# Optimization experiments

Measured on AMD Instinct MI355X. Metric: run time of the kernel, lower is better.

## Reference

```python
import jax, jax.numpy as jnp
import numpy as np
from jax.scipy.special import logsumexp

B, T, D, H, K = 64, 800, 80, 128, 39  # batch, frames, feat dim, LSTM hidden/dir, num phones


def setup_inputs() -> dict:
    key = jax.random.key(0)
    ks = jax.random.split(key, 16)
    s = 0.1
    inp = {
        "features": jax.random.normal(ks[0], (B, T, D), jnp.float32),
        "lengths": jax.random.randint(ks[1], (B,), T // 2, T + 1, dtype=jnp.int32),
        "labels": jax.random.randint(ks[2], (B, T), 0, K, dtype=jnp.int32),
        # BiLSTM params (PyTorch layout: W_ih (4H,D), W_hh (4H,H); gate order i,f,g,o)
        "Wih_f": jax.random.normal(ks[3], (4 * H, D), jnp.float32) * s,
        "Whh_f": jax.random.normal(ks[4], (4 * H, H), jnp.float32) * s,
        "bih_f": jax.random.normal(ks[5], (4 * H,), jnp.float32) * s,
        "bhh_f": jax.random.normal(ks[6], (4 * H,), jnp.float32) * s,
        "Wih_b": jax.random.normal(ks[7], (4 * H, D), jnp.float32) * s,
        "Whh_b": jax.random.normal(ks[8], (4 * H, H), jnp.float32) * s,
        "bih_b": jax.random.normal(ks[9], (4 * H,), jnp.float32) * s,
        "bhh_b": jax.random.normal(ks[10], (4 * H,), jnp.float32) * s,
        # emission projection Linear(2H -> K)
        "Wp": jax.random.normal(ks[11], (K, 2 * H), jnp.float32) * s,
        "bp": jax.random.normal(ks[12], (K,), jnp.float32) * s,
        # CRF params (pytorch-crf init: U(-0.1, 0.1))
        "start_t": jax.random.uniform(ks[13], (K,), jnp.float32, -0.1, 0.1),
        "end_t": jax.random.uniform(ks[14], (K,), jnp.float32, -0.1, 0.1),
        "trans": jax.random.uniform(ks[15], (K, K), jnp.float32, -0.1, 0.1),
    }
    return inp


def _lstm(x, Wih, Whh, bih, bhh, reverse):
    """Single-direction LSTM over padded batch. x: (B,T,D) -> (B,T,H)."""
    nB, nT, _ = x.shape
    nH = Whh.shape[1]
    xW = jnp.swapaxes(x @ Wih.T + (bih + bhh), 0, 1)  # (T,B,4H)

    def step(carry, g):
        h, c = carry
        g = g + h @ Whh.T
        i, f, gg, o = jnp.split(g, 4, axis=-1)
        c = jax.nn.sigmoid(f) * c + jax.nn.sigmoid(i) * jnp.tanh(gg)
        h = jax.nn.sigmoid(o) * jnp.tanh(c)
        return (h, c), h

    init = (jnp.zeros((nB, nH), x.dtype), jnp.zeros((nB, nH), x.dtype))
    _, hs = jax.lax.scan(step, init, xW, reverse=reverse)
    return jnp.swapaxes(hs, 0, 1)  # (B,T,H)


def _crf_nll(emissions, labels, lengths, start_t, end_t, trans):
    """pytorch-crf: -mean log-likelihood. emissions (B,T,K), labels (B,T)."""
    nB, nT, nK = emissions.shape
    mask = (jnp.arange(nT)[None, :] < lengths[:, None])  # (B,T)
    mf = mask.astype(emissions.dtype)
    bidx = jnp.arange(nB)

    # --- numerator: score of gold path ---
    num = start_t[labels[:, 0]] + emissions[bidx, 0, labels[:, 0]]
    tr = trans[labels[:, :-1], labels[:, 1:]]  # (B,T-1)
    em = jnp.take_along_axis(emissions[:, 1:], labels[:, 1:, None], axis=2)[..., 0]
    num = num + ((tr + em) * mf[:, 1:]).sum(axis=1)
    last_tags = jnp.take_along_axis(labels, (lengths - 1)[:, None], axis=1)[:, 0]
    num = num + end_t[last_tags]

    # --- denominator: forward algorithm ---
    alpha0 = start_t[None, :] + emissions[:, 0]  # (B,K)
    em_rest = jnp.swapaxes(emissions[:, 1:], 0, 1)  # (T-1,B,K)
    m_rest = jnp.swapaxes(mask[:, 1:], 0, 1)  # (T-1,B)

    def step(alpha, inputs):
        em_t, m_t = inputs
        nxt = logsumexp(alpha[:, :, None] + trans[None] + em_t[:, None, :], axis=1)
        return jnp.where(m_t[:, None], nxt, alpha), None

    alpha, _ = jax.lax.scan(step, alpha0, (em_rest, m_rest))
    denom = logsumexp(alpha + end_t[None, :], axis=1)

    return -(num - denom).mean()


def reference(features, lengths, labels, Wih_f, Whh_f, bih_f, bhh_f,
              Wih_b, Whh_b, bih_b, bhh_b, Wp, bp, start_t, end_t, trans):
    h_f = _lstm(features, Wih_f, Whh_f, bih_f, bhh_f, reverse=False)
    h_b = _lstm(features, Wih_b, Whh_b, bih_b, bhh_b, reverse=True)
    hidden = jnp.concatenate([h_f, h_b], axis=-1)  # (B,T,2H)
    emissions = hidden @ Wp.T + bp  # (B,T,K)
    return _crf_nll(emissions, labels, lengths, start_t, end_t, trans)
```

## Files before the change

### kernel.cpp

```cpp
#include <hip/hip_runtime.h>
#include <cstddef>
#include <cstdint>

#define B_ 64
#define T_ 800
#define D_ 80
#define H_ 128
#define K_ 39
#define BT_ (B_ * T_)

typedef _Float16 h2_t  __attribute__((ext_vector_type(2)));
typedef _Float16 f16x8 __attribute__((ext_vector_type(8)));
typedef float    f32x4 __attribute__((ext_vector_type(4)));
typedef uint32_t u32x4 __attribute__((ext_vector_type(4)));

__device__ __forceinline__ float fdot2_(h2_t a, h2_t b, float c) {
#if __has_builtin(__builtin_amdgcn_fdot2)
  return __builtin_amdgcn_fdot2(a, b, c, false);
#else
  return c + (float)a.x * (float)b.x + (float)a.y * (float)b.y;
#endif
}

__device__ __forceinline__ h2_t asH2u_(uint32_t u) { return __builtin_bit_cast(h2_t, u); }

__device__ __forceinline__ float sigf_(float x)  { return 1.0f / (1.0f + __expf(-x)); }
__device__ __forceinline__ float tanhf_(float x) { return 2.0f / (1.0f + __expf(-2.0f * x)) - 1.0f; }

__device__ __forceinline__ float laneb_(float v, int lane) {
  return __builtin_bit_cast(float, __builtin_amdgcn_readlane(__builtin_bit_cast(int, v), lane));
}
__device__ __forceinline__ uint32_t lanebu_(uint32_t v, int lane) {
  return (uint32_t)__builtin_amdgcn_readlane((int)v, lane);
}

__device__ __forceinline__ float dppswap1_(float v) {
  return __builtin_bit_cast(float,
    __builtin_amdgcn_mov_dpp(__builtin_bit_cast(int, v), 0xB1, 0xF, 0xF, true));
}

__device__ __forceinline__ void barrier_lds_() {
  asm volatile("s_waitcnt lgkmcnt(0)" ::: "memory");
  __builtin_amdgcn_s_barrier();
}

__device__ __forceinline__ void rows_of_(int tid, int& unit, int& role, int& r0, int& r1) {
  const int w = tid >> 6, L = tid & 63;
  unit = w * 32 + (L >> 1);
  role = L & 1;
  r0 = role * H_ + unit;
  r1 = 2 * H_ + role * H_ + unit;
}

__global__ __launch_bounds__(256, 1)
void xw_kernel(const float* __restrict__ x,
               const float* __restrict__ Wih_f, const float* __restrict__ Wih_b,
               _Float16* __restrict__ xw)
{
  const int dir = blockIdx.x & 1;
  const int mc  = blockIdx.x >> 1;
  const float* W = dir ? Wih_b : Wih_f;

  const int tid  = threadIdx.x;
  const int w    = tid >> 6;
  const int lane = tid & 63;
  const int lm   = lane & 15;
  const int quad = lane >> 4;
  const int selw = w >> 1;
  const int rolw = w & 1;

  f16x8 Bf[8][3];
  #pragma unroll
  for (int nt = 0; nt < 8; ++nt) {
    const int r = w * 128 + nt * 16 + lm;
    #pragma unroll
    for (int kt = 0; kt < 3; ++kt) {
      const int kb = kt * 32 + quad * 8;
      #pragma unroll
      for (int j = 0; j < 8; ++j) {
        const int k = kb + j;
        Bf[nt][kt][j] = (k < D_) ? (_Float16)W[(size_t)r * D_ + k] : (_Float16)0.0f;
      }
    }
  }

  __shared__ alignas(16) _Float16 xs[128 * 96];
  for (int i = tid; i < 128 * 96; i += 256) xs[i] = (_Float16)0.0f;

  for (int cc = 0; cc < 4; ++cc) {
    const int base = mc * 512 + cc * 128;
    __syncthreads();
    {
      const float4* src = (const float4*)(x + (size_t)base * D_);
      for (int i = tid; i < 128 * D_ / 4; i += 256) {
        float4 v = src[i];
        const int row = i / 20, col = (i % 20) * 4;
        h2_t p0, p1;
        p0.x = (_Float16)v.x; p0.y = (_Float16)v.y;
        p1.x = (_Float16)v.z; p1.y = (_Float16)v.w;
        uint2 pk;
        pk.x = __builtin_bit_cast(uint32_t, p0);
        pk.y = __builtin_bit_cast(uint32_t, p1);
        *(uint2*)&xs[row * 96 + col] = pk;
      }
    }
    __syncthreads();

    #pragma unroll
    for (int mt = 0; mt < 8; ++mt) {
      f16x8 Af[3];
      #pragma unroll
      for (int kt = 0; kt < 3; ++kt)
        Af[kt] = *(const f16x8*)&xs[(mt * 16 + lm) * 96 + kt * 32 + quad * 8];

      f32x4 acc[8];
      #pragma unroll
      for (int nt = 0; nt < 8; ++nt) acc[nt] = (f32x4){0.f, 0.f, 0.f, 0.f};
      #pragma unroll
      for (int kt = 0; kt < 3; ++kt)
        #pragma unroll
        for (int nt = 0; nt < 8; ++nt)
          acc[nt] = __builtin_amdgcn_mfma_f32_16x16x32_f16(Af[kt], Bf[nt][kt], acc[nt], 0, 0, 0);

      #pragma unroll
      for (int nt = 0; nt < 8; ++nt) {
        const int unit = nt * 16 + lm;
        const int ptid = (unit >> 5) * 64 + (unit & 31) * 2 + rolw;
        #pragma unroll
        for (int rg = 0; rg < 4; ++rg) {
          const int bt = base + mt * 16 + quad * 4 + rg;
          xw[((size_t)dir * BT_ + bt) * 512 + ptid * 2 + selw] = (_Float16)acc[nt][rg];
        }
      }
    }
  }
}

template<int USE_XW>
__global__ __launch_bounds__(256, 1)
void lstm_kernel(const float* __restrict__ x,
                 const float* __restrict__ Wih_f, const float* __restrict__ Whh_f,
                 const float* __restrict__ bih_f, const float* __restrict__ bhh_f,
                 const float* __restrict__ Wih_b, const float* __restrict__ Whh_b,
                 const float* __restrict__ bih_b, const float* __restrict__ bhh_b,
                 const _Float16* __restrict__ xw,
                 _Float16* __restrict__ hcat)
{
  const int bb  = blockIdx.x & 63;
  const int dir = blockIdx.x >> 6;
  const float* Whh = dir ? Whh_b : Whh_f;
  const float* Wih = dir ? Wih_b : Wih_f;
  const float* bih = dir ? bih_b : bih_f;
  const float* bhh = dir ? bhh_b : bhh_f;

  const int tid  = threadIdx.x;
  const int lane = tid & 63;
  int unit, role, r0, r1; rows_of_(tid, unit, role, r0, r1);
  const float qc1 = role ? 1.0f : 2.0f;
  const float qc0 = role ? 0.0f : -1.0f;

  h2_t w0[64], w1[64];
  #pragma unroll
  for (int j = 0; j < 64; ++j) {
    float2 a = *(const float2*)(Whh + (size_t)r0 * H_ + 2 * j);
    float2 d = *(const float2*)(Whh + (size_t)r1 * H_ + 2 * j);
    w0[j].x = (_Float16)a.x; w0[j].y = (_Float16)a.y;
    w1[j].x = (_Float16)d.x; w1[j].y = (_Float16)d.y;
  }
  h2_t wx0[40], wx1[40];
  if (!USE_XW) {
    #pragma unroll
    for (int i = 0; i < 40; ++i) {
      float2 a = *(const float2*)(Wih + (size_t)r0 * D_ + 2 * i);
      float2 d = *(const float2*)(Wih + (size_t)r1 * D_ + 2 * i);
      wx0[i].x = (_Float16)a.x; wx0[i].y = (_Float16)a.y;
      wx1[i].x = (_Float16)d.x; wx1[i].y = (_Float16)d.y;
    }
  }
  const float bias0 = bih[r0] + bhh[r0];
  const float bias1 = bih[r1] + bhh[r1];

  __shared__ alignas(16) _Float16 hsf[2][H_];
  __shared__ uint32_t xs2[2][64];

  if (tid < H_) hsf[0][tid] = (_Float16)0.0f;
  if (!USE_XW && tid < 64) { xs2[0][tid] = 0u; xs2[1][tid] = 0u; }
  float c = 0.0f;

  const uint32_t* xwdu = (const uint32_t*)xw + ((size_t)dir * BT_ + (size_t)bb * T_) * 256;
  const float*    xb   = x + (size_t)bb * T_ * D_;
  _Float16*       hb   = hcat + (size_t)bb * T_ * (2 * H_) + dir * H_;

  uint32_t xwA = 0u, xwB = 0u;
  h2_t xpend; xpend.x = (_Float16)0.f; xpend.y = (_Float16)0.f;
  {
    const int tq0 = dir ? (T_ - 1) : 0;
    const int tq1 = dir ? (T_ - 2) : 1;
    if (USE_XW) {
      xwA = xwdu[(size_t)tq0 * 256 + tid];
      xwB = xwdu[(size_t)tq1 * 256 + tid];
    } else if (tid < 40) {
      float2 v0 = *(const float2*)(xb + (size_t)tq0 * D_ + 2 * tid);
      h2_t p; p.x = (_Float16)v0.x; p.y = (_Float16)v0.y;
      xs2[0][tid] = __builtin_bit_cast(uint32_t, p);
      float2 v1 = *(const float2*)(xb + (size_t)tq1 * D_ + 2 * tid);
      xpend.x = (_Float16)v1.x; xpend.y = (_Float16)v1.y;
    }
  }
  __syncthreads();

  auto step = [&](int tt, int par, uint32_t& xwreg) {
    const int t = dir ? (T_ - 1 - tt) : tt;
    float a0, a1, b0, b1;
    if (USE_XW) {
      const h2_t xv = asH2u_(xwreg);
      a0 = bias0 + (float)xv.x;
      b0 = bias1 + (float)xv.y;
      a1 = 0.f; b1 = 0.f;
      const int ttc = (tt + 2 < T_) ? (tt + 2) : (T_ - 1);
      const int tq2 = dir ? (T_ - 1 - ttc) : ttc;
      xwreg = xwdu[(size_t)tq2 * 256 + tid];
    } else {
      a0 = bias0; a1 = 0.f; b0 = bias1; b1 = 0.f;
      if (tid < 40) {
        xs2[par ^ 1][tid] = __builtin_bit_cast(uint32_t, xpend);
        const int ttc = (tt + 2 < T_) ? (tt + 2) : (T_ - 1);
        const int tq2 = dir ? (T_ - 1 - ttc) : ttc;
        float2 v = *(const float2*)(xb + (size_t)tq2 * D_ + 2 * tid);
        xpend.x = (_Float16)v.x; xpend.y = (_Float16)v.y;
      }
      uint32_t xreg = xs2[par][lane];
      #pragma unroll
      for (int j = 0; j < 40; j += 2) {
        h2_t q0 = asH2u_(lanebu_(xreg, j));
        h2_t q1 = asH2u_(lanebu_(xreg, j + 1));
        a0 = fdot2_(wx0[j],     q0, a0); b0 = fdot2_(wx1[j],     q0, b0);
        a1 = fdot2_(wx0[j + 1], q1, a1); b1 = fdot2_(wx1[j + 1], q1, b1);
      }
    }

    const u32x4* hq = (const u32x4*)hsf[par];
    #pragma unroll
    for (int g = 0; g < 16; ++g) {
      const u32x4 hv = hq[g];
      a0 = fdot2_(w0[4 * g + 0], asH2u_(hv[0]), a0);
      b0 = fdot2_(w1[4 * g + 0], asH2u_(hv[0]), b0);
      a1 = fdot2_(w0[4 * g + 1], asH2u_(hv[1]), a1);
      b1 = fdot2_(w1[4 * g + 1], asH2u_(hv[1]), b1);
      a0 = fdot2_(w0[4 * g + 2], asH2u_(hv[2]), a0);
      b0 = fdot2_(w1[4 * g + 2], asH2u_(hv[2]), b0);
      a1 = fdot2_(w0[4 * g + 3], asH2u_(hv[3]), a1);
      b1 = fdot2_(w1[4 * g + 3], asH2u_(hv[3]), b1);
    }
    const float ga = a0 + a1;
    const float gb = b0 + b1;

    const float sg = sigf_(ga);
    const float qv = fmaf(qc1, sigf_(qc1 * gb), qc0);
    const float ex = dppswap1_(sg * qv);
    c = fmaf(sg, c, ex);
    const float hn = qv * tanhf_(c);
    if (role) {
      hsf[par ^ 1][unit] = (_Float16)hn;
      hb[(size_t)t * (2 * H_) + unit] = (_Float16)hn;
    }
    barrier_lds_();
  };

  for (int tb = 0; tb < T_; tb += 2) {
    step(tb,     0, xwA);
    step(tb + 1, 1, xwB);
  }
}

__global__ __launch_bounds__(256, 1)
void emis_kernel(const _Float16* __restrict__ hcat,
                 const float* __restrict__ Wp, const float* __restrict__ bp,
                 float* __restrict__ em)
{
  const int tid  = threadIdx.x;
  const int w    = tid >> 6;
  const int lane = tid & 63;
  const int lm   = lane & 15;
  const int quad = lane >> 4;

  f16x8 Bf[3][8];
  float bias[3];
  #pragma unroll
  for (int nt = 0; nt < 3; ++nt) {
    const int n = nt * 16 + lm;
    const bool valid = n < K_;
    bias[nt] = valid ? bp[n] : 0.0f;
    #pragma unroll
    for (int kt = 0; kt < 8; ++kt) {
      const int kb = kt * 32 + quad * 8;
      #pragma unroll
      for (int j = 0; j < 8; ++j)
        Bf[nt][kt][j] = valid ? (_Float16)Wp[(size_t)n * 256 + kb + j] : (_Float16)0.0f;
    }
  }

  #pragma unroll
  for (int q = 0; q < 4; ++q) {
    const int mt  = blockIdx.x * 16 + w * 4 + q;
    const int bt0 = mt * 16;

    f16x8 Af[8];
    const _Float16* ab = hcat + ((size_t)bt0 + lm) * 256;
    #pragma unroll
    for (int kt = 0; kt < 8; ++kt)
      Af[kt] = *(const f16x8*)(ab + kt * 32 + quad * 8);

    f32x4 acc[3];
    #pragma unroll
    for (int nt = 0; nt < 3; ++nt) acc[nt] = (f32x4){0.f, 0.f, 0.f, 0.f};
    #pragma unroll
    for (int kt = 0; kt < 8; ++kt)
      #pragma unroll
      for (int nt = 0; nt < 3; ++nt)
        acc[nt] = __builtin_amdgcn_mfma_f32_16x16x32_f16(Af[kt], Bf[nt][kt], acc[nt], 0, 0, 0);

    #pragma unroll
    for (int nt = 0; nt < 3; ++nt) {
      const int n = nt * 16 + lm;
      if (n < K_) {
        #pragma unroll
        for (int rg = 0; rg < 4; ++rg) {
          const int row = bt0 + quad * 4 + rg;
          em[(size_t)row * K_ + n] = acc[nt][rg] + bias[nt];
        }
      }
    }
  }
}

__global__ __launch_bounds__(256)
void crf_dn_kernel(const float* __restrict__ em,
                   const int* __restrict__ labels, const int* __restrict__ lengths,
                   const float* __restrict__ start_t, const float* __restrict__ end_t,
                   const float* __restrict__ trans,
                   float* __restrict__ dn)
{
  const int b    = blockIdx.x;
  const int tid  = threadIdx.x;
  const int wv   = tid >> 6;
  const int lane = tid & 63;
  const int len  = lengths[b];
  const float* emb = em + (size_t)b * T_ * K_;

  __shared__ float s_num[3];
  __shared__ float s_den;

  if (wv == 0) {
    float et[K_];
    #pragma unroll
    for (int j = 0; j < K_; ++j)
      et[j] = (lane < K_) ? __expf(trans[j * K_ + lane]) : 0.0f;

    float a0 = (lane < K_) ? (start_t[lane] + emb[lane]) : -1e30f;
    float m = a0;
    #pragma unroll
    for (int off = 32; off > 0; off >>= 1) m = fmaxf(m, __shfl_xor(m, off));
    float v = __expf(a0 - m);
    float off_acc = m;

    auto ldc = [&](int t) -> float {
      const int tc = (t < len) ? t : (len - 1);
      return (lane < K_) ? emb[(size_t)tc * K_ + lane] : 0.0f;
    };

    float eA = ldc(1), eB = ldc(2), eC = ldc(3), eD = ldc(4);
    float eE = ldc(5), eF = ldc(6), eG = ldc(7), eH = ldc(8);

    auto stepden = [&](float& ereg, int tt) {
      const float emc = ereg;
      ereg = ldc(tt + 8);
      if (tt < len) {
        const float pv = v;
        float s0 = 0.f, s1 = 0.f, s2 = 0.f, s3 = 0.f;
        #pragma unroll
        for (int j = 0; j < 36; j += 4) {
          s0 = fmaf(laneb_(pv, j),     et[j],     s0);
          s1 = fmaf(laneb_(pv, j + 1), et[j + 1], s1);
          s2 = fmaf(laneb_(pv, j + 2), et[j + 2], s2);
          s3 = fmaf(laneb_(pv, j + 3), et[j + 3], s3);
        }
        s0 = fmaf(laneb_(pv, 36), et[36], s0);
        s1 = fmaf(laneb_(pv, 37), et[37], s1);
        s2 = fmaf(laneb_(pv, 38), et[38], s2);
        v = ((s0 + s1) + (s2 + s3)) * __expf(emc);
        if ((tt & 1) == 0) {
          const float sc = laneb_(v, 0);
          v *= 1.0f / sc;
          off_acc += __logf(sc);
        }
      }
    };

    for (int t = 1; t < len; t += 8) {
      stepden(eA, t);     stepden(eB, t + 1);
      stepden(eC, t + 2); stepden(eD, t + 3);
      stepden(eE, t + 4); stepden(eF, t + 5);
      stepden(eG, t + 6); stepden(eH, t + 7);
    }

    float w = (lane < K_) ? v * __expf(end_t[lane]) : 0.0f;
    #pragma unroll
    for (int off = 32; off > 0; off >>= 1) w += __shfl_xor(w, off);
    if (lane == 0) s_den = off_acc + __logf(w);
  } else {
    const int idx = tid - 64;
    float acc = 0.0f;
    for (int t = 1 + idx; t < len; t += 192) {
      const int lp = labels[b * T_ + t - 1];
      const int lc = labels[b * T_ + t];
      acc += trans[lp * K_ + lc] + emb[(size_t)t * K_ + lc];
    }
    if (tid == 64) {
      const int l0 = labels[b * T_];
      const int ll = labels[b * T_ + len - 1];
      acc += start_t[l0] + emb[l0] + end_t[ll];
    }
    #pragma unroll
    for (int off = 32; off > 0; off >>= 1) acc += __shfl_xor(acc, off);
    if (lane == 0) s_num[wv - 1] = acc;
  }
  __syncthreads();
  if (tid == 0) dn[b] = s_den - (s_num[0] + s_num[1] + s_num[2]);
}

__global__ void finalize_kernel(const float* __restrict__ dn, float* __restrict__ out)
{
  const int tid = threadIdx.x;
  float v = dn[tid];
  #pragma unroll
  for (int off = 32; off > 0; off >>= 1) v += __shfl_down(v, off);
  if (tid == 0) out[0] = v * (1.0f / 64.0f);
}

extern "C" void kernel_launch(void* const* d_in, const int* in_sizes, int n_in,
                              void* d_out, int out_size, void* d_ws, size_t ws_size,
                              hipStream_t stream)
{
  (void)in_sizes; (void)n_in; (void)out_size;
  const float* features = (const float*)d_in[0];
  const int*   lengths  = (const int*)d_in[1];
  const int*   labels   = (const int*)d_in[2];
  const float* Wih_f = (const float*)d_in[3];
  const float* Whh_f = (const float*)d_in[4];
  const float* bih_f = (const float*)d_in[5];
  const float* bhh_f = (const float*)d_in[6];
  const float* Wih_b = (const float*)d_in[7];
  const float* Whh_b = (const float*)d_in[8];
  const float* bih_b = (const float*)d_in[9];
  const float* bhh_b = (const float*)d_in[10];
  const float* Wp      = (const float*)d_in[11];
  const float* bp      = (const float*)d_in[12];
  const float* start_t = (const float*)d_in[13];
  const float* end_t   = (const float*)d_in[14];
  const float* trans   = (const float*)d_in[15];
  float* out = (float*)d_out;

  char* wsc = (char*)d_ws;
  _Float16* hcatH = (_Float16*)wsc;
  float*    em    = (float*)(wsc + 26214400);
  float*    dn    = (float*)(wsc + 26214400 + 7987200);
  _Float16* xwH   = (_Float16*)(wsc + 34202112);
  const bool big  = ws_size >= (size_t)34202112 + 104857600;

  if (big) {
    hipLaunchKernelGGL(xw_kernel, dim3(200), dim3(256), 0, stream,
                       features, Wih_f, Wih_b, xwH);
    hipLaunchKernelGGL((lstm_kernel<1>), dim3(2 * B_), dim3(256), 0, stream,
                       features, Wih_f, Whh_f, bih_f, bhh_f,
                       Wih_b, Whh_b, bih_b, bhh_b, xwH, hcatH);
  } else {
    hipLaunchKernelGGL((lstm_kernel<0>), dim3(2 * B_), dim3(256), 0, stream,
                       features, Wih_f, Whh_f, bih_f, bhh_f,
                       Wih_b, Whh_b, bih_b, bhh_b, xwH, hcatH);
  }
  hipLaunchKernelGGL(emis_kernel, dim3(BT_ / 256), dim3(256), 0, stream,
                     hcatH, Wp, bp, em);
  hipLaunchKernelGGL(crf_dn_kernel, dim3(B_), dim3(256), 0, stream,
                     em, labels, lengths, start_t, end_t, trans, dn);
  hipLaunchKernelGGL(finalize_kernel, dim3(1), dim3(64), 0, stream,
                     dn, out);
}
```

Baseline: 777.3 us.

## Merge forward and backward LSTM directions into one 512-thread block per batch

The LSTM kernel now launches 64 blocks of 512 threads instead of 128 blocks of 256. Each block runs both directions for one batch element, with the thread index selecting the direction and shared buffers split per direction. The h-state reads from LDS are also hoisted into a register array before the dot-product loop. The block-wide barrier now couples the two directions, so each step waits for the slower half. The 512-thread blocks, each holding large per-thread weight register arrays, may also change register pressure and occupancy.

Result: slower. 1.081 ms (+39.0%).

```diff
diff --git a/kernel.cpp b/kernel.cpp
--- a/kernel.cpp
+++ b/kernel.cpp
@@ -44,8 +44,8 @@
   __builtin_amdgcn_s_barrier();
 }
 
-__device__ __forceinline__ void rows_of_(int tid, int& unit, int& role, int& r0, int& r1) {
-  const int w = tid >> 6, L = tid & 63;
+__device__ __forceinline__ void rows_of_(int tidd, int& unit, int& role, int& r0, int& r1) {
+  const int w = tidd >> 6, L = tidd & 63;
   unit = w * 32 + (L >> 1);
   role = L & 1;
   r0 = role * H_ + unit;
@@ -137,7 +137,7 @@
 }
 
 template<int USE_XW>
-__global__ __launch_bounds__(256, 1)
+__global__ __launch_bounds__(512, 1)
 void lstm_kernel(const float* __restrict__ x,
                  const float* __restrict__ Wih_f, const float* __restrict__ Whh_f,
                  const float* __restrict__ bih_f, const float* __restrict__ bhh_f,
@@ -146,16 +146,17 @@
                  const _Float16* __restrict__ xw,
                  _Float16* __restrict__ hcat)
 {
-  const int bb  = blockIdx.x & 63;
-  const int dir = blockIdx.x >> 6;
+  const int bb   = blockIdx.x;
+  const int tid  = threadIdx.x;
+  const int dir  = tid >> 8;
+  const int tidd = tid & 255;
   const float* Whh = dir ? Whh_b : Whh_f;
   const float* Wih = dir ? Wih_b : Wih_f;
   const float* bih = dir ? bih_b : bih_f;
   const float* bhh = dir ? bhh_b : bhh_f;
 
-  const int tid  = threadIdx.x;
-  const int lane = tid & 63;
-  int unit, role, r0, r1; rows_of_(tid, unit, role, r0, r1);
+  const int lane = tidd & 63;
+  int unit, role, r0, r1; rows_of_(tidd, unit, role, r0, r1);
   const float qc1 = role ? 1.0f : 2.0f;
   const float qc0 = role ? 0.0f : -1.0f;
 
@@ -180,11 +181,11 @@
   const float bias0 = bih[r0] + bhh[r0];
   const float bias1 = bih[r1] + bhh[r1];
 
-  __shared__ alignas(16) _Float16 hsf[2][H_];
-  __shared__ uint32_t xs2[2][64];
-
-  if (tid < H_) hsf[0][tid] = (_Float16)0.0f;
-  if (!USE_XW && tid < 64) { xs2[0][tid] = 0u; xs2[1][tid] = 0u; }
+  __shared__ alignas(16) _Float16 hsf[2][2][H_];
+  __shared__ uint32_t xs2[2][2][64];
+
+  if (tidd < H_) hsf[dir][0][tidd] = (_Float16)0.0f;
+  if (!USE_XW && tidd < 64) { xs2[dir][0][tidd] = 0u; xs2[dir][1][tidd] = 0u; }
   float c = 0.0f;
 
   const uint32_t* xwdu = (const uint32_t*)xw + ((size_t)dir * BT_ + (size_t)bb * T_) * 256;
@@ -197,13 +198,13 @@
     const int tq0 = dir ? (T_ - 1) : 0;
     const int tq1 = dir ? (T_ - 2) : 1;
     if (USE_XW) {
-      xwA = xwdu[(size_t)tq0 * 256 + tid];
-      xwB = xwdu[(size_t)tq1 * 256 + tid];
-    } else if (tid < 40) {
-      float2 v0 = *(const float2*)(xb + (size_t)tq0 * D_ + 2 * tid);
+      xwA = xwdu[(size_t)tq0 * 256 + tidd];
+      xwB = xwdu[(size_t)tq1 * 256 + tidd];
+    } else if (tidd < 40) {
+      float2 v0 = *(const float2*)(xb + (size_t)tq0 * D_ + 2 * tidd);
       h2_t p; p.x = (_Float16)v0.x; p.y = (_Float16)v0.y;
-      xs2[0][tid] = __builtin_bit_cast(uint32_t, p);
-      float2 v1 = *(const float2*)(xb + (size_t)tq1 * D_ + 2 * tid);
+      xs2[dir][0][tidd] = __builtin_bit_cast(uint32_t, p);
+      float2 v1 = *(const float2*)(xb + (size_t)tq1 * D_ + 2 * tidd);
       xpend.x = (_Float16)v1.x; xpend.y = (_Float16)v1.y;
     }
   }
@@ -219,17 +220,17 @@
       a1 = 0.f; b1 = 0.f;
       const int ttc = (tt + 2 < T_) ? (tt + 2) : (T_ - 1);
       const int tq2 = dir ? (T_ - 1 - ttc) : ttc;
-      xwreg = xwdu[(size_t)tq2 * 256 + tid];
+      xwreg = xwdu[(size_t)tq2 * 256 + tidd];
     } else {
       a0 = bias0; a1 = 0.f; b0 = bias1; b1 = 0.f;
-      if (tid < 40) {
-        xs2[par ^ 1][tid] = __builtin_bit_cast(uint32_t, xpend);
+      if (tidd < 40) {
+        xs2[dir][par ^ 1][tidd] = __builtin_bit_cast(uint32_t, xpend);
         const int ttc = (tt + 2 < T_) ? (tt + 2) : (T_ - 1);
         const int tq2 = dir ? (T_ - 1 - ttc) : ttc;
-        float2 v = *(const float2*)(xb + (size_t)tq2 * D_ + 2 * tid);
+        float2 v = *(const float2*)(xb + (size_t)tq2 * D_ + 2 * tidd);
         xpend.x = (_Float16)v.x; xpend.y = (_Float16)v.y;
       }
-      uint32_t xreg = xs2[par][lane];
+      uint32_t xreg = xs2[dir][par][lane];
       #pragma unroll
       for (int j = 0; j < 40; j += 2) {
         h2_t q0 = asH2u_(lanebu_(xreg, j));
@@ -239,18 +240,20 @@
       }
     }
 
-    const u32x4* hq = (const u32x4*)hsf[par];
+    const u32x4* hq = (const u32x4*)hsf[dir][par];
+    u32x4 hvv[16];
+    #pragma unroll
+    for (int g = 0; g < 16; ++g) hvv[g] = hq[g];
     #pragma unroll
     for (int g = 0; g < 16; ++g) {
-      const u32x4 hv = hq[g];
-      a0 = fdot2_(w0[4 * g + 0], asH2u_(hv[0]), a0);
-      b0 = fdot2_(w1[4 * g + 0], asH2u_(hv[0]), b0);
-      a1 = fdot2_(w0[4 * g + 1], asH2u_(hv[1]), a1);
-      b1 = fdot2_(w1[4 * g + 1], asH2u_(hv[1]), b1);
-      a0 = fdot2_(w0[4 * g + 2], asH2u_(hv[2]), a0);
-      b0 = fdot2_(w1[4 * g + 2], asH2u_(hv[2]), b0);
-      a1 = fdot2_(w0[4 * g + 3], asH2u_(hv[3]), a1);
-      b1 = fdot2_(w1[4 * g + 3], asH2u_(hv[3]), b1);
+      a0 = fdot2_(w0[4 * g + 0], asH2u_(hvv[g][0]), a0);
+      b0 = fdot2_(w1[4 * g + 0], asH2u_(hvv[g][0]), b0);
+      a1 = fdot2_(w0[4 * g + 1], asH2u_(hvv[g][1]), a1);
+      b1 = fdot2_(w1[4 * g + 1], asH2u_(hvv[g][1]), b1);
+      a0 = fdot2_(w0[4 * g + 2], asH2u_(hvv[g][2]), a0);
+      b0 = fdot2_(w1[4 * g + 2], asH2u_(hvv[g][2]), b0);
+      a1 = fdot2_(w0[4 * g + 3], asH2u_(hvv[g][3]), a1);
+      b1 = fdot2_(w1[4 * g + 3], asH2u_(hvv[g][3]), b1);
     }
     const float ga = a0 + a1;
     const float gb = b0 + b1;
@@ -261,7 +264,7 @@
     c = fmaf(sg, c, ex);
     const float hn = qv * tanhf_(c);
     if (role) {
-      hsf[par ^ 1][unit] = (_Float16)hn;
+      hsf[dir][par ^ 1][unit] = (_Float16)hn;
       hb[(size_t)t * (2 * H_) + unit] = (_Float16)hn;
     }
     barrier_lds_();
@@ -471,11 +474,11 @@
   if (big) {
     hipLaunchKernelGGL(xw_kernel, dim3(200), dim3(256), 0, stream,
                        features, Wih_f, Wih_b, xwH);
-    hipLaunchKernelGGL((lstm_kernel<1>), dim3(2 * B_), dim3(256), 0, stream,
+    hipLaunchKernelGGL((lstm_kernel<1>), dim3(B_), dim3(512), 0, stream,
                        features, Wih_f, Whh_f, bih_f, bhh_f,
                        Wih_b, Whh_b, bih_b, bhh_b, xwH, hcatH);
   } else {
-    hipLaunchKernelGGL((lstm_kernel<0>), dim3(2 * B_), dim3(256), 0, stream,
+    hipLaunchKernelGGL((lstm_kernel<0>), dim3(B_), dim3(512), 0, stream,
                        features, Wih_f, Whh_f, bih_f, bhh_f,
                        Wih_b, Whh_b, bih_b, bhh_b, xwH, hcatH);
   }
```

## Batch LSTM recurrence over 16 sequences per block using MFMA

Applied to the files above, without the earlier changes.

Replaces the per-sequence fdot2 LSTM recurrence (128 blocks, one batch element per direction) with an MFMA-based kernel. Each of 8 blocks of 512 threads handles 16 batch elements for one direction and computes the h@Whh^T gate product with 16x16x32 f16 MFMAs, keeping the weights in registers. The xw precompute output layout is rearranged to match the new per-timestep tile loads, and the gate nonlinearities are rewritten with clamped exps and hardware reciprocals. This uses only 8 CUs where the old kernel used 128, trading parallel width for far fewer instructions per step, so the serial per-step latency (MFMA chain plus barrier) now sets the runtime.

Result: slower. 1.148 ms (+47.7%).

```diff
diff --git a/kernel.cpp b/kernel.cpp
--- a/kernel.cpp
+++ b/kernel.cpp
@@ -10,9 +10,9 @@
 #define BT_ (B_ * T_)
 
 typedef _Float16 h2_t  __attribute__((ext_vector_type(2)));
+typedef _Float16 h4_t  __attribute__((ext_vector_type(4)));
 typedef _Float16 f16x8 __attribute__((ext_vector_type(8)));
 typedef float    f32x4 __attribute__((ext_vector_type(4)));
-typedef uint32_t u32x4 __attribute__((ext_vector_type(4)));
 
 __device__ __forceinline__ float fdot2_(h2_t a, h2_t b, float c) {
 #if __has_builtin(__builtin_amdgcn_fdot2)
@@ -27,6 +27,14 @@
 __device__ __forceinline__ float sigf_(float x)  { return 1.0f / (1.0f + __expf(-x)); }
 __device__ __forceinline__ float tanhf_(float x) { return 2.0f / (1.0f + __expf(-2.0f * x)) - 1.0f; }
 
+__device__ __forceinline__ float rcpf_(float x) {
+#if __has_builtin(__builtin_amdgcn_rcpf)
+  return __builtin_amdgcn_rcpf(x);
+#else
+  return 1.0f / x;
+#endif
+}
+
 __device__ __forceinline__ float laneb_(float v, int lane) {
   return __builtin_bit_cast(float, __builtin_amdgcn_readlane(__builtin_bit_cast(int, v), lane));
 }
@@ -66,8 +74,6 @@
   const int lane = tid & 63;
   const int lm   = lane & 15;
   const int quad = lane >> 4;
-  const int selw = w >> 1;
-  const int rolw = w & 1;
 
   f16x8 Bf[8][3];
   #pragma unroll
@@ -122,28 +128,150 @@
         for (int nt = 0; nt < 8; ++nt)
           acc[nt] = __builtin_amdgcn_mfma_f32_16x16x32_f16(Af[kt], Bf[nt][kt], acc[nt], 0, 0, 0);
 
+      int tA[4], bA[4];
+      #pragma unroll
+      for (int rg = 0; rg < 4; ++rg) {
+        const int bt = base + mt * 16 + quad * 4 + rg;
+        bA[rg] = bt / T_;
+        tA[rg] = bt % T_;
+      }
       #pragma unroll
       for (int nt = 0; nt < 8; ++nt) {
-        const int unit = nt * 16 + lm;
-        const int ptid = (unit >> 5) * 64 + (unit & 31) * 2 + rolw;
         #pragma unroll
         for (int rg = 0; rg < 4; ++rg) {
-          const int bt = base + mt * 16 + quad * 4 + rg;
-          xw[((size_t)dir * BT_ + bt) * 512 + ptid * 2 + selw] = (_Float16)acc[nt][rg];
+          const size_t addr = (size_t)(tA[rg] * 2 + dir) * 32768
+                            + (size_t)(w * 8 + nt) * 1024
+                            + (size_t)(lm >> 2) * 256
+                            + (size_t)bA[rg] * 4 + (lm & 3);
+          xw[addr] = (_Float16)acc[nt][rg];
         }
       }
     }
   }
 }
 
-template<int USE_XW>
+__global__ __launch_bounds__(512, 1)
+void lstm_mfma_kernel(const _Float16* __restrict__ xwN,
+                      const float* __restrict__ Whh_f, const float* __restrict__ Whh_b,
+                      const float* __restrict__ bih_f, const float* __restrict__ bhh_f,
+                      const float* __restrict__ bih_b, const float* __restrict__ bhh_b,
+                      _Float16* __restrict__ hcat)
+{
+  const int d  = blockIdx.x & 1;
+  const int bg = blockIdx.x >> 1;
+  const float* Whh = d ? Whh_b : Whh_f;
+  const float* bih = d ? bih_b : bih_f;
+  const float* bhh = d ? bhh_b : bhh_f;
+
+  const int tid  = threadIdx.x;
+  const int w    = tid >> 6;
+  const int lane = tid & 63;
+  const int lm   = lane & 15;
+  const int quad = lane >> 4;
+  const int bglob = bg * 16 + lm;
+  const int u0   = w * 16 + quad * 4;
+
+  f16x8 Af[4][4];
+  #pragma unroll
+  for (int ti = 0; ti < 4; ++ti) {
+    const int gr = (w + 8 * ti) * 16 + lm;
+    #pragma unroll
+    for (int ks = 0; ks < 4; ++ks) {
+      const float* src = Whh + (size_t)gr * H_ + ks * 32 + quad * 8;
+      #pragma unroll
+      for (int j = 0; j < 8; ++j) Af[ti][ks][j] = (_Float16)src[j];
+    }
+  }
+  float bias[4][4];
+  #pragma unroll
+  for (int ti = 0; ti < 4; ++ti) {
+    #pragma unroll
+    for (int r = 0; r < 4; ++r) {
+      const int gr = (w + 8 * ti) * 16 + quad * 4 + r;
+      bias[ti][r] = bih[gr] + bhh[gr];
+    }
+  }
+
+  __shared__ alignas(16) _Float16 hT[2][16][136];
+  for (int i = tid; i < 2 * 16 * 136; i += 512) (&hT[0][0][0])[i] = (_Float16)0.0f;
+  float c[4] = {0.f, 0.f, 0.f, 0.f};
+
+  auto ldxq = [&](int t, h4_t* xq) {
+    const _Float16* p = xwN + (size_t)(t * 2 + d) * 32768
+                      + (size_t)quad * 256 + (size_t)bglob * 4;
+    #pragma unroll
+    for (int ti = 0; ti < 4; ++ti)
+      xq[ti] = *(const h4_t*)(p + (size_t)(w + 8 * ti) * 1024);
+  };
+
+  h4_t xqA[4], xqB[4];
+  ldxq(d ? (T_ - 1) : 0, xqA);
+  ldxq(d ? (T_ - 2) : 1, xqB);
+  __syncthreads();
+
+  auto step = [&](int tt, int par, h4_t* xq) {
+    const int t = d ? (T_ - 1 - tt) : tt;
+
+    f32x4 acc[4];
+    #pragma unroll
+    for (int ti = 0; ti < 4; ++ti)
+      #pragma unroll
+      for (int r = 0; r < 4; ++r)
+        acc[ti][r] = bias[ti][r] + (float)xq[ti][r];
+
+    {
+      const int ttc = (tt + 2 < T_) ? (tt + 2) : (T_ - 1);
+      const int tq  = d ? (T_ - 1 - ttc) : ttc;
+      ldxq(tq, xq);
+    }
+
+    f16x8 Bf[4];
+    #pragma unroll
+    for (int ks = 0; ks < 4; ++ks)
+      Bf[ks] = *(const f16x8*)&hT[par][lm][ks * 32 + quad * 8];
+
+    #pragma unroll
+    for (int ks = 0; ks < 4; ++ks)
+      #pragma unroll
+      for (int ti = 0; ti < 4; ++ti)
+        acc[ti] = __builtin_amdgcn_mfma_f32_16x16x32_f16(Af[ti][ks], Bf[ks], acc[ti], 0, 0, 0);
+
+    h4_t hh;
+    #pragma unroll
+    for (int r = 0; r < 4; ++r) {
+      const float gi = acc[0][r], gf = acc[1][r], gg = acc[2][r], go = acc[3][r];
+      const float ei  = __expf(-gi);
+      const float gcl = fminf(fmaxf(gg, -12.f), 12.f);
+      const float eg  = __expf(-2.f * gcl);
+      const float ef  = __expf(-gf);
+      const float eo  = __expf(-go);
+      const float sitg = (1.f - eg) * rcpf_((1.f + ei) * (1.f + eg));
+      const float sf   = rcpf_(1.f + ef);
+      const float cn   = fmaf(sf, c[r], sitg);
+      c[r] = cn;
+      const float ccl = fminf(fmaxf(cn, -12.f), 12.f);
+      const float ec  = __expf(-2.f * ccl);
+      const float h   = (1.f - ec) * rcpf_((1.f + eo) * (1.f + ec));
+      hh[r] = (_Float16)h;
+    }
+
+    *(h4_t*)&hT[par ^ 1][lm][u0] = hh;
+    *(h4_t*)(hcat + ((size_t)bglob * T_ + t) * 256 + d * 128 + u0) = hh;
+    barrier_lds_();
+  };
+
+  for (int tb = 0; tb < T_; tb += 2) {
+    step(tb,     0, xqA);
+    step(tb + 1, 1, xqB);
+  }
+}
+
 __global__ __launch_bounds__(256, 1)
-void lstm_kernel(const float* __restrict__ x,
+void lstm_fallback_kernel(const float* __restrict__ x,
                  const float* __restrict__ Wih_f, const float* __restrict__ Whh_f,
                  const float* __restrict__ bih_f, const float* __restrict__ bhh_f,
                  const float* __restrict__ Wih_b, const float* __restrict__ Whh_b,
                  const float* __restrict__ bih_b, const float* __restrict__ bhh_b,
-                 const _Float16* __restrict__ xw,
                  _Float16* __restrict__ hcat)
 {
   const int bb  = blockIdx.x & 63;
@@ -168,38 +296,31 @@
     w1[j].x = (_Float16)d.x; w1[j].y = (_Float16)d.y;
   }
   h2_t wx0[40], wx1[40];
-  if (!USE_XW) {
-    #pragma unroll
-    for (int i = 0; i < 40; ++i) {
-      float2 a = *(const float2*)(Wih + (size_t)r0 * D_ + 2 * i);
-      float2 d = *(const float2*)(Wih + (size_t)r1 * D_ + 2 * i);
-      wx0[i].x = (_Float16)a.x; wx0[i].y = (_Float16)a.y;
-      wx1[i].x = (_Float16)d.x; wx1[i].y = (_Float16)d.y;
-    }
+  #pragma unroll
+  for (int i = 0; i < 40; ++i) {
+    float2 a = *(const float2*)(Wih + (size_t)r0 * D_ + 2 * i);
+    float2 d = *(const float2*)(Wih + (size_t)r1 * D_ + 2 * i);
+    wx0[i].x = (_Float16)a.x; wx0[i].y = (_Float16)a.y;
+    wx1[i].x = (_Float16)d.x; wx1[i].y = (_Float16)d.y;
   }
   const float bias0 = bih[r0] + bhh[r0];
   const float bias1 = bih[r1] + bhh[r1];
 
-  __shared__ alignas(16) _Float16 hsf[2][H_];
+  __shared__ alignas(8) _Float16 hsf[2][H_];
   __shared__ uint32_t xs2[2][64];
 
   if (tid < H_) hsf[0][tid] = (_Float16)0.0f;
-  if (!USE_XW && tid < 64) { xs2[0][tid] = 0u; xs2[1][tid] = 0u; }
+  if (tid < 64) { xs2[0][tid] = 0u; xs2[1][tid] = 0u; }
   float c = 0.0f;
 
-  const uint32_t* xwdu = (const uint32_t*)xw + ((size_t)dir * BT_ + (size_t)bb * T_) * 256;
-  const float*    xb   = x + (size_t)bb * T_ * D_;
-  _Float16*       hb   = hcat + (size_t)bb * T_ * (2 * H_) + dir * H_;
-
-  uint32_t xwA = 0u, xwB = 0u;
+  const float* xb = x + (size_t)bb * T_ * D_;
+  _Float16*    hb = hcat + (size_t)bb * T_ * (2 * H_) + dir * H_;
+
   h2_t xpend; xpend.x = (_Float16)0.f; xpend.y = (_Float16)0.f;
   {
     const int tq0 = dir ? (T_ - 1) : 0;
     const int tq1 = dir ? (T_ - 2) : 1;
-    if (USE_XW) {
-      xwA = xwdu[(size_t)tq0 * 256 + tid];
-      xwB = xwdu[(size_t)tq1 * 256 + tid];
-    } else if (tid < 40) {
+    if (tid < 40) {
       float2 v0 = *(const float2*)(xb + (size_t)tq0 * D_ + 2 * tid);
       h2_t p; p.x = (_Float16)v0.x; p.y = (_Float16)v0.y;
       xs2[0][tid] = __builtin_bit_cast(uint32_t, p);
@@ -209,52 +330,34 @@
   }
   __syncthreads();
 
-  auto step = [&](int tt, int par, uint32_t& xwreg) {
+  auto step = [&](int tt, int par) {
     const int t = dir ? (T_ - 1 - tt) : tt;
-    float a0, a1, b0, b1;
-    if (USE_XW) {
-      const h2_t xv = asH2u_(xwreg);
-      a0 = bias0 + (float)xv.x;
-      b0 = bias1 + (float)xv.y;
-      a1 = 0.f; b1 = 0.f;
+    float a0 = bias0, a1 = 0.f, b0 = bias1, b1 = 0.f;
+    if (tid < 40) {
+      xs2[par ^ 1][tid] = __builtin_bit_cast(uint32_t, xpend);
       const int ttc = (tt + 2 < T_) ? (tt + 2) : (T_ - 1);
       const int tq2 = dir ? (T_ - 1 - ttc) : ttc;
-      xwreg = xwdu[(size_t)tq2 * 256 + tid];
-    } else {
-      a0 = bias0; a1 = 0.f; b0 = bias1; b1 = 0.f;
-      if (tid < 40) {
-        xs2[par ^ 1][tid] = __builtin_bit_cast(uint32_t, xpend);
-        const int ttc = (tt + 2 < T_) ? (tt + 2) : (T_ - 1);
-        const int tq2 = dir ? (T_ - 1 - ttc) : ttc;
-        float2 v = *(const float2*)(xb + (size_t)tq2 * D_ + 2 * tid);
-        xpend.x = (_Float16)v.x; xpend.y = (_Float16)v.y;
-      }
-      uint32_t xreg = xs2[par][lane];
-      #pragma unroll
-      for (int j = 0; j < 40; j += 2) {
-        h2_t q0 = asH2u_(lanebu_(xreg, j));
-        h2_t q1 = asH2u_(lanebu_(xreg, j + 1));
-        a0 = fdot2_(wx0[j],     q0, a0); b0 = fdot2_(wx1[j],     q0, b0);
-        a1 = fdot2_(wx0[j + 1], q1, a1); b1 = fdot2_(wx1[j + 1], q1, b1);
-      }
-    }
-
-    const u32x4* hq = (const u32x4*)hsf[par];
-    #pragma unroll
-    for (int g = 0; g < 16; ++g) {
-      const u32x4 hv = hq[g];
-      a0 = fdot2_(w0[4 * g + 0], asH2u_(hv[0]), a0);
-      b0 = fdot2_(w1[4 * g + 0], asH2u_(hv[0]), b0);
-      a1 = fdot2_(w0[4 * g + 1], asH2u_(hv[1]), a1);
-      b1 = fdot2_(w1[4 * g + 1], asH2u_(hv[1]), b1);
-      a0 = fdot2_(w0[4 * g + 2], asH2u_(hv[2]), a0);
-      b0 = fdot2_(w1[4 * g + 2], asH2u_(hv[2]), b0);
-      a1 = fdot2_(w0[4 * g + 3], asH2u_(hv[3]), a1);
-      b1 = fdot2_(w1[4 * g + 3], asH2u_(hv[3]), b1);
+      float2 v = *(const float2*)(xb + (size_t)tq2 * D_ + 2 * tid);
+      xpend.x = (_Float16)v.x; xpend.y = (_Float16)v.y;
+    }
+    uint32_t xreg = xs2[par][lane];
+    #pragma unroll
+    for (int j = 0; j < 40; j += 2) {
+      h2_t q0 = asH2u_(lanebu_(xreg, j));
+      h2_t q1 = asH2u_(lanebu_(xreg, j + 1));
+      a0 = fdot2_(wx0[j],     q0, a0); b0 = fdot2_(wx1[j],     q0, b0);
+      a1 = fdot2_(wx0[j + 1], q1, a1); b1 = fdot2_(wx1[j + 1], q1, b1);
+    }
+    const uint32_t* hq = (const uint32_t*)hsf[par];
+    #pragma unroll
+    for (int g = 0; g < 64; g += 2) {
+      h2_t hv0 = asH2u_(hq[g]);
+      h2_t hv1 = asH2u_(hq[g + 1]);
+      a0 = fdot2_(w0[g],     hv0, a0); b0 = fdot2_(w1[g],     hv0, b0);
+      a1 = fdot2_(w0[g + 1], hv1, a1); b1 = fdot2_(w1[g + 1], hv1, b1);
     }
     const float ga = a0 + a1;
     const float gb = b0 + b1;
-
     const float sg = sigf_(ga);
     const float qv = fmaf(qc1, sigf_(qc1 * gb), qc0);
     const float ex = dppswap1_(sg * qv);
@@ -268,8 +371,8 @@
   };
 
   for (int tb = 0; tb < T_; tb += 2) {
-    step(tb,     0, xwA);
-    step(tb + 1, 1, xwB);
+    step(tb, 0);
+    step(tb + 1, 1);
   }
 }
 
@@ -471,13 +574,12 @@
   if (big) {
     hipLaunchKernelGGL(xw_kernel, dim3(200), dim3(256), 0, stream,
                        features, Wih_f, Wih_b, xwH);
-    hipLaunchKernelGGL((lstm_kernel<1>), dim3(2 * B_), dim3(256), 0, stream,
+    hipLaunchKernelGGL(lstm_mfma_kernel, dim3(8), dim3(512), 0, stream,
+                       xwH, Whh_f, Whh_b, bih_f, bhh_f, bih_b, bhh_b, hcatH);
+  } else {
+    hipLaunchKernelGGL(lstm_fallback_kernel, dim3(2 * B_), dim3(256), 0, stream,
                        features, Wih_f, Whh_f, bih_f, bhh_f,
-                       Wih_b, Whh_b, bih_b, bhh_b, xwH, hcatH);
-  } else {
-    hipLaunchKernelGGL((lstm_kernel<0>), dim3(2 * B_), dim3(256), 0, stream,
-                       features, Wih_f, Whh_f, bih_f, bhh_f,
-                       Wih_b, Whh_b, bih_b, bhh_b, xwH, hcatH);
+                       Wih_b, Whh_b, bih_b, bhh_b, hcatH);
   }
   hipLaunchKernelGGL(emis_kernel, dim3(BT_ / 256), dim3(256), 0, stream,
                      hcatH, Wp, bp, em);
```

## Prescale LSTM weights by -log2e, use exp2/rcp gates, LDS broadcast in CRF

Applied to the files above, without the earlier changes.

Folds the -log2(e) factor (or -2·log2(e) for the g gate) into the input and recurrent weights and biases. Sigmoid and tanh then become exp2 plus reciprocal, with no extra multiply on the serial recurrence path. The recurrent dot products are split over four accumulators instead of two to shorten dependency chains. Time-index pointers now advance incrementally rather than being recomputed each step. In the CRF forward pass, per-lane readlane broadcasts are replaced by an LDS write and vectorized float4 reads, which adds an LDS round trip per step. Scaling the weights before the fp16 conversion changes rounding slightly.

Result: no change. 788.8 us (+1.5%).

```diff
diff --git a/kernel.cpp b/kernel.cpp
--- a/kernel.cpp
+++ b/kernel.cpp
@@ -9,6 +9,9 @@
 #define K_ 39
 #define BT_ (B_ * T_)
 
+#define NL2E_  (-1.44269504f)
+#define N2L2E_ (-2.88539008f)
+
 typedef _Float16 h2_t  __attribute__((ext_vector_type(2)));
 typedef _Float16 f16x8 __attribute__((ext_vector_type(8)));
 typedef float    f32x4 __attribute__((ext_vector_type(4)));
@@ -24,7 +27,20 @@
 
 __device__ __forceinline__ h2_t asH2u_(uint32_t u) { return __builtin_bit_cast(h2_t, u); }
 
-__device__ __forceinline__ float sigf_(float x)  { return 1.0f / (1.0f + __expf(-x)); }
+__device__ __forceinline__ float ex2_(float x) {
+#if __has_builtin(__builtin_amdgcn_exp2f)
+  return __builtin_amdgcn_exp2f(x);
+#else
+  return __builtin_exp2f(x);
+#endif
+}
+__device__ __forceinline__ float rcpf_(float x) {
+#if __has_builtin(__builtin_amdgcn_rcpf)
+  return __builtin_amdgcn_rcpf(x);
+#else
+  return 1.0f / x;
+#endif
+}
 __device__ __forceinline__ float tanhf_(float x) { return 2.0f / (1.0f + __expf(-2.0f * x)) - 1.0f; }
 
 __device__ __forceinline__ float laneb_(float v, int lane) {
@@ -73,13 +89,14 @@
   #pragma unroll
   for (int nt = 0; nt < 8; ++nt) {
     const int r = w * 128 + nt * 16 + lm;
+    const float fac = (r >= 256 && r < 384) ? N2L2E_ : NL2E_;
     #pragma unroll
     for (int kt = 0; kt < 3; ++kt) {
       const int kb = kt * 32 + quad * 8;
       #pragma unroll
       for (int j = 0; j < 8; ++j) {
         const int k = kb + j;
-        Bf[nt][kt][j] = (k < D_) ? (_Float16)W[(size_t)r * D_ + k] : (_Float16)0.0f;
+        Bf[nt][kt][j] = (k < D_) ? (_Float16)(fac * W[(size_t)r * D_ + k]) : (_Float16)0.0f;
       }
     }
   }
@@ -156,16 +173,17 @@
   const int tid  = threadIdx.x;
   const int lane = tid & 63;
   int unit, role, r0, r1; rows_of_(tid, unit, role, r0, r1);
-  const float qc1 = role ? 1.0f : 2.0f;
-  const float qc0 = role ? 0.0f : -1.0f;
+  const float s0 = NL2E_;
+  const float s1 = role ? NL2E_ : N2L2E_;
+  const float qk2 = role ? 0.0f : -1.0f;
 
   h2_t w0[64], w1[64];
   #pragma unroll
   for (int j = 0; j < 64; ++j) {
     float2 a = *(const float2*)(Whh + (size_t)r0 * H_ + 2 * j);
     float2 d = *(const float2*)(Whh + (size_t)r1 * H_ + 2 * j);
-    w0[j].x = (_Float16)a.x; w0[j].y = (_Float16)a.y;
-    w1[j].x = (_Float16)d.x; w1[j].y = (_Float16)d.y;
+    w0[j].x = (_Float16)(s0 * a.x); w0[j].y = (_Float16)(s0 * a.y);
+    w1[j].x = (_Float16)(s1 * d.x); w1[j].y = (_Float16)(s1 * d.y);
   }
   h2_t wx0[40], wx1[40];
   if (!USE_XW) {
@@ -173,12 +191,12 @@
     for (int i = 0; i < 40; ++i) {
       float2 a = *(const float2*)(Wih + (size_t)r0 * D_ + 2 * i);
       float2 d = *(const float2*)(Wih + (size_t)r1 * D_ + 2 * i);
-      wx0[i].x = (_Float16)a.x; wx0[i].y = (_Float16)a.y;
-      wx1[i].x = (_Float16)d.x; wx1[i].y = (_Float16)d.y;
-    }
-  }
-  const float bias0 = bih[r0] + bhh[r0];
-  const float bias1 = bih[r1] + bhh[r1];
+      wx0[i].x = (_Float16)(s0 * a.x); wx0[i].y = (_Float16)(s0 * a.y);
+      wx1[i].x = (_Float16)(s1 * d.x); wx1[i].y = (_Float16)(s1 * d.y);
+    }
+  }
+  const float bias0 = s0 * (bih[r0] + bhh[r0]);
+  const float bias1 = s1 * (bih[r1] + bhh[r1]);
 
   __shared__ alignas(16) _Float16 hsf[2][H_];
   __shared__ uint32_t xs2[2][64];
@@ -190,6 +208,11 @@
   const uint32_t* xwdu = (const uint32_t*)xw + ((size_t)dir * BT_ + (size_t)bb * T_) * 256;
   const float*    xb   = x + (size_t)bb * T_ * D_;
   _Float16*       hb   = hcat + (size_t)bb * T_ * (2 * H_) + dir * H_;
+
+  _Float16* hbp = hb + (size_t)(dir ? (T_ - 1) : 0) * (2 * H_);
+  const ptrdiff_t hstep = dir ? -(2 * H_) : (2 * H_);
+  int xoff = (dir ? (T_ - 3) : 2) * 256 + tid;
+  const int xstep = dir ? -256 : 256;
 
   uint32_t xwA = 0u, xwB = 0u;
   h2_t xpend; xpend.x = (_Float16)0.f; xpend.y = (_Float16)0.f;
@@ -210,18 +233,16 @@
   __syncthreads();
 
   auto step = [&](int tt, int par, uint32_t& xwreg) {
-    const int t = dir ? (T_ - 1 - tt) : tt;
-    float a0, a1, b0, b1;
+    float a0, a1, a2, a3, b0, b1, b2, b3;
     if (USE_XW) {
       const h2_t xv = asH2u_(xwreg);
       a0 = bias0 + (float)xv.x;
       b0 = bias1 + (float)xv.y;
-      a1 = 0.f; b1 = 0.f;
-      const int ttc = (tt + 2 < T_) ? (tt + 2) : (T_ - 1);
-      const int tq2 = dir ? (T_ - 1 - ttc) : ttc;
-      xwreg = xwdu[(size_t)tq2 * 256 + tid];
+      a1 = a2 = a3 = 0.f; b1 = b2 = b3 = 0.f;
+      xwreg = xwdu[xoff];
     } else {
-      a0 = bias0; a1 = 0.f; b0 = bias1; b1 = 0.f;
+      a0 = bias0; b0 = bias1;
+      a1 = a2 = a3 = 0.f; b1 = b2 = b3 = 0.f;
       if (tid < 40) {
         xs2[par ^ 1][tid] = __builtin_bit_cast(uint32_t, xpend);
         const int ttc = (tt + 2 < T_) ? (tt + 2) : (T_ - 1);
@@ -231,11 +252,15 @@
       }
       uint32_t xreg = xs2[par][lane];
       #pragma unroll
-      for (int j = 0; j < 40; j += 2) {
+      for (int j = 0; j < 40; j += 4) {
         h2_t q0 = asH2u_(lanebu_(xreg, j));
         h2_t q1 = asH2u_(lanebu_(xreg, j + 1));
+        h2_t q2 = asH2u_(lanebu_(xreg, j + 2));
+        h2_t q3 = asH2u_(lanebu_(xreg, j + 3));
         a0 = fdot2_(wx0[j],     q0, a0); b0 = fdot2_(wx1[j],     q0, b0);
         a1 = fdot2_(wx0[j + 1], q1, a1); b1 = fdot2_(wx1[j + 1], q1, b1);
+        a2 = fdot2_(wx0[j + 2], q2, a2); b2 = fdot2_(wx1[j + 2], q2, b2);
+        a3 = fdot2_(wx0[j + 3], q3, a3); b3 = fdot2_(wx1[j + 3], q3, b3);
       }
     }
 
@@ -247,23 +272,28 @@
       b0 = fdot2_(w1[4 * g + 0], asH2u_(hv[0]), b0);
       a1 = fdot2_(w0[4 * g + 1], asH2u_(hv[1]), a1);
       b1 = fdot2_(w1[4 * g + 1], asH2u_(hv[1]), b1);
-      a0 = fdot2_(w0[4 * g + 2], asH2u_(hv[2]), a0);
-      b0 = fdot2_(w1[4 * g + 2], asH2u_(hv[2]), b0);
-      a1 = fdot2_(w0[4 * g + 3], asH2u_(hv[3]), a1);
-      b1 = fdot2_(w1[4 * g + 3], asH2u_(hv[3]), b1);
-    }
-    const float ga = a0 + a1;
-    const float gb = b0 + b1;
-
-    const float sg = sigf_(ga);
-    const float qv = fmaf(qc1, sigf_(qc1 * gb), qc0);
+      a2 = fdot2_(w0[4 * g + 2], asH2u_(hv[2]), a2);
+      b2 = fdot2_(w1[4 * g + 2], asH2u_(hv[2]), b2);
+      a3 = fdot2_(w0[4 * g + 3], asH2u_(hv[3]), a3);
+      b3 = fdot2_(w1[4 * g + 3], asH2u_(hv[3]), b3);
+    }
+    const float ga = (a0 + a1) + (a2 + a3);
+    const float gb = (b0 + b1) + (b2 + b3);
+
+    const float ea = ex2_(ga);
+    const float sg = rcpf_(1.0f + ea);
+    const float gbc = fminf(fmaxf(gb, -34.6f), 34.6f);
+    const float eb = ex2_(gbc);
+    const float qv = fmaf(qk2, eb, 1.0f) * rcpf_(1.0f + eb);
     const float ex = dppswap1_(sg * qv);
     c = fmaf(sg, c, ex);
     const float hn = qv * tanhf_(c);
     if (role) {
       hsf[par ^ 1][unit] = (_Float16)hn;
-      hb[(size_t)t * (2 * H_) + unit] = (_Float16)hn;
-    }
+      hbp[unit] = (_Float16)hn;
+    }
+    hbp += hstep;
+    if (tt + 3 < T_) xoff += xstep;
     barrier_lds_();
   };
 
@@ -350,6 +380,7 @@
 
   __shared__ float s_num[3];
   __shared__ float s_den;
+  __shared__ alignas(16) float vbuf[64];
 
   if (wv == 0) {
     float et[K_];
@@ -363,6 +394,7 @@
     for (int off = 32; off > 0; off >>= 1) m = fmaxf(m, __shfl_xor(m, off));
     float v = __expf(a0 - m);
     float off_acc = m;
+    vbuf[lane] = 0.0f;
 
     auto ldc = [&](int t) -> float {
       const int tc = (t < len) ? t : (len - 1);
@@ -376,18 +408,22 @@
       const float emc = ereg;
       ereg = ldc(tt + 8);
       if (tt < len) {
-        const float pv = v;
+        vbuf[lane] = v;
+        asm volatile("s_waitcnt lgkmcnt(0)" ::: "memory");
+        const float4* vq = (const float4*)vbuf;
         float s0 = 0.f, s1 = 0.f, s2 = 0.f, s3 = 0.f;
         #pragma unroll
-        for (int j = 0; j < 36; j += 4) {
-          s0 = fmaf(laneb_(pv, j),     et[j],     s0);
-          s1 = fmaf(laneb_(pv, j + 1), et[j + 1], s1);
-          s2 = fmaf(laneb_(pv, j + 2), et[j + 2], s2);
-          s3 = fmaf(laneb_(pv, j + 3), et[j + 3], s3);
+        for (int g = 0; g < 9; ++g) {
+          const float4 q = vq[g];
+          s0 = fmaf(q.x, et[4 * g],     s0);
+          s1 = fmaf(q.y, et[4 * g + 1], s1);
+          s2 = fmaf(q.z, et[4 * g + 2], s2);
+          s3 = fmaf(q.w, et[4 * g + 3], s3);
         }
-        s0 = fmaf(laneb_(pv, 36), et[36], s0);
-        s1 = fmaf(laneb_(pv, 37), et[37], s1);
-        s2 = fmaf(laneb_(pv, 38), et[38], s2);
+        const float4 q9 = vq[9];
+        s0 = fmaf(q9.x, et[36], s0);
+        s1 = fmaf(q9.y, et[37], s1);
+        s2 = fmaf(q9.z, et[38], s2);
         v = ((s0 + s1) + (s2 + s3)) * __expf(emc);
         if ((tt & 1) == 0) {
           const float sc = laneb_(v, 0);
```
